# Optimization experiments

Measured on AMD Instinct MI355X. Metric: run time of the kernel, lower is better.

Reference implementation:

```python
import jax, jax.numpy as jnp
import numpy as np
import math

INPUT_SIZE = 64  # feature dim D, matches init_kwargs input_size


def setup_inputs() -> dict:
    key = jax.random.key(0)
    k1, k2 = jax.random.split(key)
    B, N, D = 32, 2048, INPUT_SIZE
    x = jax.random.normal(k1, (B, N, D), dtype=jnp.float32)
    adj = jax.random.randint(k2, (N, N), 0, 2, dtype=jnp.int32)
    return {"input": x, "adj": adj}


def reference(input, adj):
    # input: [B, N, D], adj: [N, N]
    scale = 1.0 / math.sqrt(INPUT_SIZE)
    # batched QK^T: [B, N, N]
    scores = jnp.einsum('bnd,bmd->bnm', input, input) * scale
    neg = jnp.float32(-1e12)
    masked = jnp.where(adj > 0, scores, neg)  # adj broadcasts over batch
    attn = jax.nn.softmax(masked, axis=-1)
    # AV: [B, N, D]
    out = jnp.einsum('bnm,bmd->bnd', attn, input)
    return out
```

## Files before the change

kernel.cpp:

```cpp
#include <hip/hip_runtime.h>
#include <hip/hip_bf16.h>

#define NB 32
#define NN 2048
#define DD 64
#define NCH 32
#define LOG2E 1.44269504088896340736f
#define SQC 0.4246613965f

typedef __attribute__((ext_vector_type(8))) short short8;
typedef __attribute__((ext_vector_type(4))) short short4v;
typedef __attribute__((ext_vector_type(4))) float f32x4;

#define MFMA32K(A, B, C) \
  __builtin_amdgcn_mfma_f32_16x16x32_bf16((A), (B), (C), 0, 0, 0)
#define MFMA16(A, B, C) \
  __builtin_amdgcn_mfma_f32_16x16x16bf16_1k((A), (B), (C), 0, 0, 0)

#define GLOAD_LDS16(gp, lp)                                                   \
  __builtin_amdgcn_global_load_lds(                                          \
      (const __attribute__((address_space(1))) void*)(gp),                   \
      (__attribute__((address_space(3))) void*)(lp), 16, 0, 0)

__device__ __forceinline__ short f2bf(float x) {
  __bf16 h = (__bf16)x;
  return __builtin_bit_cast(short, h);
}

__device__ __forceinline__ float fast_exp2(float x) {
#if __has_builtin(__builtin_amdgcn_exp2f)
  return __builtin_amdgcn_exp2f(x);
#else
  return exp2f(x);
#endif
}

__device__ __forceinline__ unsigned pack_bf16_rnd(float lo, float hi) {
  unsigned ulo = __builtin_bit_cast(unsigned, lo) + 0x8000u;
  unsigned uhi = __builtin_bit_cast(unsigned, hi) + 0x8000u;
  return __builtin_amdgcn_perm(uhi, ulo, 0x07060302u);
}

__global__ __launch_bounds__(256) void prep_img(const float* __restrict__ x,
                                                short* __restrict__ img) {
  __shared__ float t[64 * 68];
  const int tid = threadIdx.x;
  const int c = blockIdx.x;
  const int b = blockIdx.y;
  const int r = tid >> 2;
  const int cg = tid & 3;

  const float* src = x + ((size_t)b * NN + c * 64 + r) * DD + cg * 16;
#pragma unroll
  for (int h = 0; h < 4; ++h)
    *(float4*)&t[r * 68 + cg * 16 + h * 4] = ((const float4*)src)[h];
  __syncthreads();

  short* imgc = img + (size_t)(b * NCH + c) * 16 * 512;

#pragma unroll
  for (int i = 0; i < 2; ++i) {
    const int kc = tid + i * 256;
    const int u = kc >> 6, l = kc & 63;
    const int nt = u >> 1, ks = u & 1;
    const float* tr = &t[(nt * 16 + (l & 15)) * 68 + ks * 32 + (l >> 4) * 8];
    short8 v;
#pragma unroll
    for (int j = 0; j < 8; ++j) v[j] = f2bf(tr[j] * SQC);
    *(short8*)&imgc[(size_t)u * 512 + l * 8] = v;
  }
#pragma unroll
  for (int i = 0; i < 2; ++i) {
    const int vc = tid + i * 256;
    const int u = vc >> 6, l = vc & 63;
    const int dt = u >> 1, ntp = u & 1;
    const int d = dt * 16 + (l & 15);
    const int k0 = ntp * 32 + ((l >> 4) << 2);
    short8 o;
#pragma unroll
    for (int h = 0; h < 2; ++h)
#pragma unroll
      for (int r2 = 0; r2 < 4; ++r2)
        o[h * 4 + r2] = f2bf(t[(k0 + h * 16 + r2) * 68 + d]);
    *(short8*)&imgc[(size_t)(8 + u) * 512 + l * 8] = o;
  }
}

__global__ __launch_bounds__(256) void prep_adj(const int* __restrict__ adj,
                                                unsigned long long* __restrict__ bits) {
  const int i = blockIdx.x * 256 + threadIdx.x;
  unsigned long long m = __ballot(adj[i] > 0);
  if ((threadIdx.x & 63) == 0) bits[i >> 6] = m;
}

__global__ __launch_bounds__(128, 2) void gat_flash9(
    const short* __restrict__ img, const unsigned long long* __restrict__ adjb,
    float* __restrict__ out) {
  __shared__ short sI[2][8192];

  const int beta = blockIdx.x;
  const int xcd = beta & 7;
  const int idx = beta >> 3;
  const int bb = idx >> 5;
  const int xq = idx & 31;
  const int b = xcd * 4 + bb;

  const int tid = threadIdx.x;
  const int w = tid >> 6;
  const int l = tid & 63;
  const int lane16 = l & 15;
  const int quad = l >> 4;
  const int qbase = xq * 64 + w * 32;
  const int coff = idx & 31;

  const short* img_b = img + (size_t)b * NCH * 8192;

  short8 qf[2][2];
#pragma unroll
  for (int qt = 0; qt < 2; ++qt)
#pragma unroll
    for (int ks = 0; ks < 2; ++ks)
      qf[qt][ks] = *(const short8*)&img_b[((size_t)xq * 16 +
                                          (w * 2 + qt) * 2 + ks) * 512 + l * 8];

  f32x4 acc[2][4];
  f32x4 acl[2];
#pragma unroll
  for (int qt = 0; qt < 2; ++qt) {
    acl[qt] = {0.f, 0.f, 0.f, 0.f};
#pragma unroll
    for (int dt = 0; dt < 4; ++dt) acc[qt][dt] = {0.f, 0.f, 0.f, 0.f};
  }
  short4v ones;
  ones[0] = 0x3F80; ones[1] = 0x3F80; ones[2] = 0x3F80; ones[3] = 0x3F80;
  const f32x4 zero = {0.f, 0.f, 0.f, 0.f};

  const unsigned long long* ar0 = adjb + (size_t)(qbase + lane16) * NCH;
  const unsigned long long* ar1 = adjb + (size_t)(qbase + 16 + lane16) * NCH;

  {
    const short* p = img_b + (size_t)coff * 8192;
#pragma unroll
    for (int i = 0; i < 8; ++i) {
      const int u = i * 2 + w;
      GLOAD_LDS16(p + (size_t)u * 512 + l * 8, &sI[0][u * 512]);
    }
  }
  __syncthreads();

  for (int ci = 0; ci < NCH; ++ci) {
    const int c = (ci + coff) & 31;
    const int cur = ci & 1;
    if (ci < NCH - 1) {
      const int cn = (ci + 1 + coff) & 31;
      const short* p = img_b + (size_t)cn * 8192;
#pragma unroll
      for (int i = 0; i < 8; ++i) {
        const int u = i * 2 + w;
        GLOAD_LDS16(p + (size_t)u * 512 + l * 8, &sI[cur ^ 1][u * 512]);
      }
    }

    const unsigned long long a0 = ar0[c] >> (quad * 4);
    const unsigned long long a1 = ar1[c] >> (quad * 4);
    const unsigned m0[2] = {(unsigned)a0, (unsigned)(a0 >> 32)};
    const unsigned m1[2] = {(unsigned)a1, (unsigned)(a1 >> 32)};

    const short* sKc = sI[cur];
    const short* sVc = sI[cur] + 4096;

    f32x4 sS[2][2];
    {
      short8 k0 = *(const short8*)&sKc[0 * 512 + l * 8];
      short8 k1 = *(const short8*)&sKc[1 * 512 + l * 8];
      sS[0][0] = MFMA32K(k0, qf[0][0], zero);
      sS[0][0] = MFMA32K(k1, qf[0][1], sS[0][0]);
      sS[0][1] = MFMA32K(k0, qf[1][0], zero);
      sS[0][1] = MFMA32K(k1, qf[1][1], sS[0][1]);
    }

    short8 vv[4];
#pragma unroll
    for (int nt = 0; nt < 4; ++nt) {
      const int pp = nt & 1;
      if (nt < 3) {
        short8 k0 = *(const short8*)&sKc[((nt + 1) * 2) * 512 + l * 8];
        short8 k1 = *(const short8*)&sKc[((nt + 1) * 2 + 1) * 512 + l * 8];
        sS[pp ^ 1][0] = MFMA32K(k0, qf[0][0], zero);
        sS[pp ^ 1][0] = MFMA32K(k1, qf[0][1], sS[pp ^ 1][0]);
        sS[pp ^ 1][1] = MFMA32K(k0, qf[1][0], zero);
        sS[pp ^ 1][1] = MFMA32K(k1, qf[1][1], sS[pp ^ 1][1]);
      }
      if (pp == 0) {
#pragma unroll
        for (int dt = 0; dt < 4; ++dt)
          vv[dt] = *(const short8*)&sVc[(dt * 2 + (nt >> 1)) * 512 + l * 8];
      }
      const unsigned w0 = m0[nt >> 1], w1 = m1[nt >> 1];
      const int sh = pp * 16;
      float p0[4], p1[4];
#pragma unroll
      for (int r = 0; r < 4; ++r) {
        float e0 = fast_exp2(sS[pp][0][r]);
        float e1 = fast_exp2(sS[pp][1][r]);
        p0[r] = ((w0 >> (sh + r)) & 1u) ? e0 : 0.f;
        p1[r] = ((w1 >> (sh + r)) & 1u) ? e1 : 0.f;
      }
      uint2 u0, u1;
      u0.x = pack_bf16_rnd(p0[0], p0[1]);
      u0.y = pack_bf16_rnd(p0[2], p0[3]);
      u1.x = pack_bf16_rnd(p1[0], p1[1]);
      u1.y = pack_bf16_rnd(p1[2], p1[3]);
      short4v pf0 = __builtin_bit_cast(short4v, u0);
      short4v pf1 = __builtin_bit_cast(short4v, u1);
      acl[0] = MFMA16(ones, pf0, acl[0]);
      acl[1] = MFMA16(ones, pf1, acl[1]);
#pragma unroll
      for (int dt = 0; dt < 4; ++dt) {
        short4v vh = (pp == 0)
                         ? __builtin_shufflevector(vv[dt], vv[dt], 0, 1, 2, 3)
                         : __builtin_shufflevector(vv[dt], vv[dt], 4, 5, 6, 7);
        acc[0][dt] = MFMA16(vh, pf0, acc[0][dt]);
        acc[1][dt] = MFMA16(vh, pf1, acc[1][dt]);
      }
    }
    __syncthreads();
  }

#pragma unroll
  for (int qt = 0; qt < 2; ++qt) {
    const float inv = 1.0f / acl[qt][0];
    float* op =
        out + ((size_t)b * NN + qbase + qt * 16 + lane16) * DD + quad * 4;
#pragma unroll
    for (int dt = 0; dt < 4; ++dt) {
      float4 o;
      o.x = acc[qt][dt][0] * inv;
      o.y = acc[qt][dt][1] * inv;
      o.z = acc[qt][dt][2] * inv;
      o.w = acc[qt][dt][3] * inv;
      *(float4*)(op + dt * 16) = o;
    }
  }
}

extern "C" void kernel_launch(void* const* d_in, const int* in_sizes, int n_in,
                              void* d_out, int out_size, void* d_ws,
                              size_t ws_size, hipStream_t stream) {
  const float* x = (const float*)d_in[0];
  const int* adj = (const int*)d_in[1];
  float* out = (float*)d_out;

  short* img = (short*)d_ws;
  unsigned long long* adjb =
      (unsigned long long*)(img + (size_t)NB * NCH * 16 * 512);

  prep_img<<<dim3(NCH, NB), 256, 0, stream>>>(x, img);
  prep_adj<<<(NN * NN) / 256, 256, 0, stream>>>(adj, adjb);
  gat_flash9<<<1024, 128, 0, stream>>>(img, adjb, out);
}
```

Before: 152.2 us.

## Restage P through per-wave LDS to use K=32 MFMA for PV, drop shared K/V staging

Changes the PV product from 16x16x16 MFMAs fed directly from registers to 16x16x32 MFMAs, writing the probability tile into a per-wave LDS scratch so it can be reloaded in the wider operand layout. The V image layout in the prep kernel changes to match. The row-sum MFMA against a ones vector is replaced by scalar accumulation and cross-lane shuffles. K/V chunks are now read straight from global memory into registers, with no shared double buffer or block barrier. Blocks grow to 4 waves covering 128 queries, with a staggered chunk start. This halves the PV MFMA count and removes block-wide synchronisation, at the cost of an LDS round-trip per chunk and more reliance on L2 for K/V reuse.

```diff
diff --git a/kernel.cpp b/kernel.cpp
--- a/kernel.cpp
+++ b/kernel.cpp
@@ -14,13 +14,6 @@
 
 #define MFMA32K(A, B, C) \
   __builtin_amdgcn_mfma_f32_16x16x32_bf16((A), (B), (C), 0, 0, 0)
-#define MFMA16(A, B, C) \
-  __builtin_amdgcn_mfma_f32_16x16x16bf16_1k((A), (B), (C), 0, 0, 0)
-
-#define GLOAD_LDS16(gp, lp)                                                   \
-  __builtin_amdgcn_global_load_lds(                                          \
-      (const __attribute__((address_space(1))) void*)(gp),                   \
-      (__attribute__((address_space(3))) void*)(lp), 16, 0, 0)
 
 __device__ __forceinline__ short f2bf(float x) {
   __bf16 h = (__bf16)x;
@@ -73,15 +66,12 @@
   for (int i = 0; i < 2; ++i) {
     const int vc = tid + i * 256;
     const int u = vc >> 6, l = vc & 63;
-    const int dt = u >> 1, ntp = u & 1;
+    const int dt = u >> 1, win = u & 1;
     const int d = dt * 16 + (l & 15);
-    const int k0 = ntp * 32 + ((l >> 4) << 2);
+    const int key0 = win * 32 + (l >> 4) * 8;
     short8 o;
 #pragma unroll
-    for (int h = 0; h < 2; ++h)
-#pragma unroll
-      for (int r2 = 0; r2 < 4; ++r2)
-        o[h * 4 + r2] = f2bf(t[(k0 + h * 16 + r2) * 68 + d]);
+    for (int j = 0; j < 8; ++j) o[j] = f2bf(t[(key0 + j) * 68 + d]);
     *(short8*)&imgc[(size_t)(8 + u) * 512 + l * 8] = o;
   }
 }
@@ -93,16 +83,16 @@
   if ((threadIdx.x & 63) == 0) bits[i >> 6] = m;
 }
 
-__global__ __launch_bounds__(128, 2) void gat_flash9(
+__global__ __launch_bounds__(256, 2) void gat_flash10(
     const short* __restrict__ img, const unsigned long long* __restrict__ adjb,
     float* __restrict__ out) {
-  __shared__ short sI[2][8192];
+  __shared__ short sP[4 * 2048];
 
   const int beta = blockIdx.x;
   const int xcd = beta & 7;
   const int idx = beta >> 3;
-  const int bb = idx >> 5;
-  const int xq = idx & 31;
+  const int bb = idx >> 4;
+  const int xq = idx & 15;
   const int b = xcd * 4 + bb;
 
   const int tid = threadIdx.x;
@@ -110,126 +100,97 @@
   const int l = tid & 63;
   const int lane16 = l & 15;
   const int quad = l >> 4;
-  const int qbase = xq * 64 + w * 32;
-  const int coff = idx & 31;
+  const int qbase = xq * 128 + w * 32;
+  const int coff = (idx * 11) & 31;
 
   const short* img_b = img + (size_t)b * NCH * 8192;
-
+  short* sPw = sP + w * 2048;
+
+  const int qc = xq * 2 + (w >> 1);
   short8 qf[2][2];
 #pragma unroll
   for (int qt = 0; qt < 2; ++qt)
 #pragma unroll
     for (int ks = 0; ks < 2; ++ks)
-      qf[qt][ks] = *(const short8*)&img_b[((size_t)xq * 16 +
-                                          (w * 2 + qt) * 2 + ks) * 512 + l * 8];
+      qf[qt][ks] = *(const short8*)&img_b[((size_t)qc * 16 +
+                                          ((w & 1) * 2 + qt) * 2 + ks) * 512 +
+                                          l * 8];
 
   f32x4 acc[2][4];
-  f32x4 acl[2];
-#pragma unroll
-  for (int qt = 0; qt < 2; ++qt) {
-    acl[qt] = {0.f, 0.f, 0.f, 0.f};
+#pragma unroll
+  for (int qt = 0; qt < 2; ++qt)
 #pragma unroll
     for (int dt = 0; dt < 4; ++dt) acc[qt][dt] = {0.f, 0.f, 0.f, 0.f};
-  }
-  short4v ones;
-  ones[0] = 0x3F80; ones[1] = 0x3F80; ones[2] = 0x3F80; ones[3] = 0x3F80;
+  float lpart[2] = {0.f, 0.f};
   const f32x4 zero = {0.f, 0.f, 0.f, 0.f};
 
   const unsigned long long* ar0 = adjb + (size_t)(qbase + lane16) * NCH;
   const unsigned long long* ar1 = adjb + (size_t)(qbase + 16 + lane16) * NCH;
 
-  {
-    const short* p = img_b + (size_t)coff * 8192;
-#pragma unroll
-    for (int i = 0; i < 8; ++i) {
-      const int u = i * 2 + w;
-      GLOAD_LDS16(p + (size_t)u * 512 + l * 8, &sI[0][u * 512]);
-    }
-  }
-  __syncthreads();
-
   for (int ci = 0; ci < NCH; ++ci) {
-    const int c = (ci + coff) & 31;
-    const int cur = ci & 1;
-    if (ci < NCH - 1) {
-      const int cn = (ci + 1 + coff) & 31;
-      const short* p = img_b + (size_t)cn * 8192;
-#pragma unroll
-      for (int i = 0; i < 8; ++i) {
-        const int u = i * 2 + w;
-        GLOAD_LDS16(p + (size_t)u * 512 + l * 8, &sI[cur ^ 1][u * 512]);
-      }
-    }
-
-    const unsigned long long a0 = ar0[c] >> (quad * 4);
-    const unsigned long long a1 = ar1[c] >> (quad * 4);
+    const int cc = (ci + coff) & 31;
+    const short* gc = img_b + (size_t)cc * 8192;
+
+    short8 kf[8], vf[8];
+#pragma unroll
+    for (int u = 0; u < 8; ++u) kf[u] = *(const short8*)&gc[u * 512 + l * 8];
+#pragma unroll
+    for (int u = 0; u < 8; ++u)
+      vf[u] = *(const short8*)&gc[(8 + u) * 512 + l * 8];
+
+    const unsigned long long a0 = ar0[cc] >> (quad * 4);
+    const unsigned long long a1 = ar1[cc] >> (quad * 4);
     const unsigned m0[2] = {(unsigned)a0, (unsigned)(a0 >> 32)};
     const unsigned m1[2] = {(unsigned)a1, (unsigned)(a1 >> 32)};
 
-    const short* sKc = sI[cur];
-    const short* sVc = sI[cur] + 4096;
-
-    f32x4 sS[2][2];
-    {
-      short8 k0 = *(const short8*)&sKc[0 * 512 + l * 8];
-      short8 k1 = *(const short8*)&sKc[1 * 512 + l * 8];
-      sS[0][0] = MFMA32K(k0, qf[0][0], zero);
-      sS[0][0] = MFMA32K(k1, qf[0][1], sS[0][0]);
-      sS[0][1] = MFMA32K(k0, qf[1][0], zero);
-      sS[0][1] = MFMA32K(k1, qf[1][1], sS[0][1]);
-    }
-
-    short8 vv[4];
 #pragma unroll
     for (int nt = 0; nt < 4; ++nt) {
-      const int pp = nt & 1;
-      if (nt < 3) {
-        short8 k0 = *(const short8*)&sKc[((nt + 1) * 2) * 512 + l * 8];
-        short8 k1 = *(const short8*)&sKc[((nt + 1) * 2 + 1) * 512 + l * 8];
-        sS[pp ^ 1][0] = MFMA32K(k0, qf[0][0], zero);
-        sS[pp ^ 1][0] = MFMA32K(k1, qf[0][1], sS[pp ^ 1][0]);
-        sS[pp ^ 1][1] = MFMA32K(k0, qf[1][0], zero);
-        sS[pp ^ 1][1] = MFMA32K(k1, qf[1][1], sS[pp ^ 1][1]);
-      }
-      if (pp == 0) {
-#pragma unroll
-        for (int dt = 0; dt < 4; ++dt)
-          vv[dt] = *(const short8*)&sVc[(dt * 2 + (nt >> 1)) * 512 + l * 8];
-      }
+      f32x4 s0 = MFMA32K(kf[nt * 2], qf[0][0], zero);
+      s0 = MFMA32K(kf[nt * 2 + 1], qf[0][1], s0);
+      f32x4 s1 = MFMA32K(kf[nt * 2], qf[1][0], zero);
+      s1 = MFMA32K(kf[nt * 2 + 1], qf[1][1], s1);
+
       const unsigned w0 = m0[nt >> 1], w1 = m1[nt >> 1];
-      const int sh = pp * 16;
+      const int sh = (nt & 1) * 16;
       float p0[4], p1[4];
 #pragma unroll
       for (int r = 0; r < 4; ++r) {
-        float e0 = fast_exp2(sS[pp][0][r]);
-        float e1 = fast_exp2(sS[pp][1][r]);
+        float e0 = fast_exp2(s0[r]);
+        float e1 = fast_exp2(s1[r]);
         p0[r] = ((w0 >> (sh + r)) & 1u) ? e0 : 0.f;
         p1[r] = ((w1 >> (sh + r)) & 1u) ? e1 : 0.f;
+        lpart[0] += p0[r];
+        lpart[1] += p1[r];
       }
       uint2 u0, u1;
       u0.x = pack_bf16_rnd(p0[0], p0[1]);
       u0.y = pack_bf16_rnd(p0[2], p0[3]);
       u1.x = pack_bf16_rnd(p1[0], p1[1]);
       u1.y = pack_bf16_rnd(p1[2], p1[3]);
-      short4v pf0 = __builtin_bit_cast(short4v, u0);
-      short4v pf1 = __builtin_bit_cast(short4v, u1);
-      acl[0] = MFMA16(ones, pf0, acl[0]);
-      acl[1] = MFMA16(ones, pf1, acl[1]);
-#pragma unroll
-      for (int dt = 0; dt < 4; ++dt) {
-        short4v vh = (pp == 0)
-                         ? __builtin_shufflevector(vv[dt], vv[dt], 0, 1, 2, 3)
-                         : __builtin_shufflevector(vv[dt], vv[dt], 4, 5, 6, 7);
-        acc[0][dt] = MFMA16(vh, pf0, acc[0][dt]);
-        acc[1][dt] = MFMA16(vh, pf1, acc[1][dt]);
+      const int win = nt >> 1;
+      const int lq = ((nt & 1) * 2 + (quad >> 1)) * 16 + lane16;
+      const int off = lq * 8 + (quad & 1) * 4;
+      *(short4v*)&sPw[(win * 2 + 0) * 512 + off] = __builtin_bit_cast(short4v, u0);
+      *(short4v*)&sPw[(win * 2 + 1) * 512 + off] = __builtin_bit_cast(short4v, u1);
+    }
+
+#pragma unroll
+    for (int win = 0; win < 2; ++win)
+#pragma unroll
+      for (int qt = 0; qt < 2; ++qt) {
+        short8 pfrag = *(const short8*)&sPw[(win * 2 + qt) * 512 + l * 8];
+#pragma unroll
+        for (int dt = 0; dt < 4; ++dt)
+          acc[qt][dt] = MFMA32K(vf[dt * 2 + win], pfrag, acc[qt][dt]);
       }
-    }
-    __syncthreads();
   }
 
 #pragma unroll
   for (int qt = 0; qt < 2; ++qt) {
-    const float inv = 1.0f / acl[qt][0];
+    float lq = lpart[qt];
+    lq += __shfl_xor(lq, 16, 64);
+    lq += __shfl_xor(lq, 32, 64);
+    const float inv = 1.0f / lq;
     float* op =
         out + ((size_t)b * NN + qbase + qt * 16 + lane16) * DD + quad * 4;
 #pragma unroll
@@ -257,5 +218,5 @@
 
   prep_img<<<dim3(NCH, NB), 256, 0, stream>>>(x, img);
   prep_adj<<<(NN * NN) / 256, 256, 0, stream>>>(adj, adjb);
-  gat_flash9<<<1024, 128, 0, stream>>>(img, adjb, out);
-}
+  gat_flash10<<<512, 256, 0, stream>>>(img, adjb, out);
+}
```

Measured after the change: 150.7 us. No clear change (-1.0%).
